# Optimization experiments

Hardware: AMD Instinct MI355X
Metric: run time of the kernel (lower is better)

## Reference

```python
import jax, jax.numpy as jnp
import numpy as np

N_NODES = 50000
N_EDGES = 800000
HIDDEN = 128
STATIC = 16
EDGE_F = 16
HEADS = 8
HEAD_SIZE = HIDDEN // HEADS
MLP_IN = 2 * HIDDEN + 2 * STATIC + EDGE_F  # 304
MLP_WIDTH = 2 * HIDDEN  # 256


def setup_inputs() -> dict:
    key = jax.random.key(0)
    ks = jax.random.split(key, 7)
    h = jax.random.normal(ks[0], (N_NODES, HIDDEN), dtype=jnp.float32)
    x_s = jax.random.normal(ks[1], (N_NODES, STATIC), dtype=jnp.float32)
    edge_index = jax.random.randint(ks[2], (2, N_EDGES), 0, N_NODES, dtype=jnp.int32)
    edge_features = jax.random.normal(ks[3], (N_EDGES, EDGE_F), dtype=jnp.float32)
    W1 = jax.random.normal(ks[4], (MLP_WIDTH, MLP_IN), dtype=jnp.float32) / np.sqrt(MLP_IN)
    W2 = jax.random.normal(ks[5], (HEADS, MLP_WIDTH), dtype=jnp.float32) / np.sqrt(MLP_WIDTH)
    Wout = jax.random.normal(ks[6], (HIDDEN, HIDDEN), dtype=jnp.float32) / np.sqrt(HIDDEN)
    return {"h": h, "x_s": x_s, "edge_index": edge_index,
            "edge_features": edge_features, "W1": W1, "W2": W2, "Wout": Wout}


def reference(h, x_s, edge_index, edge_features, W1, W2, Wout):
    num_nodes, hidden = h.shape
    # original does edge_index[::-1] -> src = edge_index[1], dest = edge_index[0]
    src, dest = edge_index[1], edge_index[0]
    # per-edge gate MLP (depth=1, relu hidden, no bias)
    mlp_input = jnp.concatenate([h[src], h[dest], x_s[src], x_s[dest], edge_features], axis=-1)  # [E, 304]
    hidden_act = jax.nn.relu(mlp_input @ W1.T)          # [E, width]
    raw_scores = hidden_act @ W2.T                      # [E, heads]
    gates = jax.nn.sigmoid(raw_scores)                  # [E, heads]
    # head-split gather-multiply-scatter
    h_heads = h.reshape(num_nodes, HEADS, HEAD_SIZE)
    gated = h_heads[src] * gates[:, :, None]            # [E, heads, head_size]
    agg = jax.ops.segment_sum(gated, dest, num_segments=num_nodes)  # [N, heads, head_size]
    agg = agg.reshape(num_nodes, hidden)
    projected = agg @ Wout.T                            # [N, hidden]
    return (projected, gates)
```

## Files before the change

### kernel.cpp

```cpp
#include <hip/hip_runtime.h>
#include <hip/hip_bf16.h>

#define N_NODES 50000
#define N_EDGES 800000
#define HIDDEN 128
#define STATIC 16
#define EDGE_F 16
#define HEADS 8
#define KIN 304
#define KPAD 320
#define WID 256
#define TILE 64
#define NTILES (N_EDGES / TILE)
#define NB 512

typedef short bf16x8 __attribute__((ext_vector_type(8)));
typedef unsigned short u16x4 __attribute__((ext_vector_type(4)));
typedef unsigned short u16x8 __attribute__((ext_vector_type(8)));
typedef float f32x4 __attribute__((ext_vector_type(4)));

__device__ __forceinline__ unsigned short f2bf(float x) {
    __hip_bfloat16 b = __float2bfloat16(x);
    return __builtin_bit_cast(unsigned short, b);
}

__global__ void prep_weights_kernel(const float* __restrict__ W1,
                                    const float* __restrict__ W2,
                                    unsigned short* __restrict__ wb1p,
                                    unsigned short* __restrict__ wb2p) {
    int gi = blockIdx.x * 256 + threadIdx.x;
    if (gi < WID * (KPAD / 8)) {
        int row = gi / 40, kg = gi - row * 40;
        u16x8 o = (u16x8)0;
        if (kg < 38) {
            const float* s = W1 + (size_t)row * KIN + kg * 8;
            #pragma unroll
            for (int i = 0; i < 8; ++i) o[i] = f2bf(s[i]);
        }
        *(u16x8*)(wb1p + (size_t)gi * 8) = o;
    } else {
        int gj = gi - WID * (KPAD / 8);
        if (gj < 16 * 32) {
            int row = gj >> 5, kg = gj & 31;
            u16x8 o = (u16x8)0;
            if (row < HEADS) {
                const float* s = W2 + (size_t)row * WID + kg * 8;
                #pragma unroll
                for (int i = 0; i < 8; ++i) o[i] = f2bf(s[i]);
            }
            *(u16x8*)(wb2p + (size_t)gj * 8) = o;
        }
    }
}

#define HB_G  (N_NODES * HIDDEN / 8)
#define XSB_G (N_NODES * STATIC / 8)
#define EFB_G (N_EDGES * EDGE_F / 8)
__global__ void prep_data_kernel(const float* __restrict__ h,
                                 const float* __restrict__ xs,
                                 const float* __restrict__ ef,
                                 unsigned short* __restrict__ hb,
                                 unsigned short* __restrict__ xsb,
                                 unsigned short* __restrict__ efb) {
    size_t gi = (size_t)blockIdx.x * 256 + threadIdx.x;
    const float* s;
    unsigned short* d;
    if (gi < HB_G)                    { s = h  + gi * 8;              d = hb  + gi * 8; }
    else if (gi < HB_G + XSB_G)       { size_t k = gi - HB_G;         s = xs + k * 8; d = xsb + k * 8; }
    else if (gi < HB_G + XSB_G + EFB_G) { size_t k = gi - HB_G - XSB_G; s = ef + k * 8; d = efb + k * 8; }
    else return;
    u16x8 o;
    #pragma unroll
    for (int i = 0; i < 8; ++i) o[i] = f2bf(s[i]);
    *(u16x8*)d = o;
}

template <bool PRE>
__global__ __launch_bounds__(256, 2) void mlp_gates_kernel(
    const float* __restrict__ hf, const float* __restrict__ xsf,
    const int* __restrict__ ei, const float* __restrict__ eff,
    const unsigned short* __restrict__ wb1p, const unsigned short* __restrict__ wb2p,
    const unsigned short* __restrict__ hb, const unsigned short* __restrict__ xsb,
    const unsigned short* __restrict__ efb,
    float* __restrict__ gates_out)
{
    __shared__ __align__(16) short A_sh[TILE * KPAD];
    __shared__ __align__(16) short hid_sh[TILE * WID];
    __shared__ int src_s[TILE], dst_s[TILE];

    const int tid  = threadIdx.x;
    const int lane = tid & 63;
    const int w    = tid >> 6;
    const int r    = lane & 15;
    const int g    = lane >> 4;
    const int xorv = (r & 7) << 4;

    bf16x8 b1[4][10];
    #pragma unroll
    for (int t = 0; t < 4; ++t)
        #pragma unroll
        for (int ks = 0; ks < 10; ++ks)
            b1[t][ks] = *(const bf16x8*)(wb1p + (size_t)((w * 4 + t) * 16 + r) * KPAD + ks * 32 + g * 8);
    bf16x8 w2f[8];
    #pragma unroll
    for (int k2 = 0; k2 < 8; ++k2)
        w2f[k2] = *(const bf16x8*)(wb2p + (size_t)r * WID + k2 * 32 + g * 8);

    int tile = blockIdx.x;
    if (tid < TILE && tile < NTILES) {
        src_s[tid] = ei[N_EDGES + tile * TILE + tid];
        dst_s[tid] = ei[tile * TILE + tid];
    }
    __syncthreads();

    for (; tile < NTILES; tile += NB) {
        const int e0 = tile * TILE;

        if (PRE) {
            const u16x8* h8  = (const u16x8*)hb;
            const u16x8* xs8 = (const u16x8*)xsb;
            const u16x8* ef8 = (const u16x8*)efb;
            #pragma unroll
            for (int idx = tid; idx < 1024; idx += 256) {
                int e = idx >> 4, c = idx & 15;
                u16x8 v = h8[(size_t)src_s[e] * 16 + c];
                *(u16x8*)((char*)A_sh + e * 640 + (((c << 4)) ^ ((e & 7) << 4))) = v;
            }
            #pragma unroll
            for (int idx = tid; idx < 1024; idx += 256) {
                int e = idx >> 4, c = idx & 15;
                u16x8 v = h8[(size_t)dst_s[e] * 16 + c];
                *(u16x8*)((char*)A_sh + e * 640 + ((256 + (c << 4)) ^ ((e & 7) << 4))) = v;
            }
            #pragma unroll
            for (int idx = tid; idx < 512; idx += 256) {
                int e = idx >> 3, c = idx & 7;
                u16x8 v = (u16x8)0;
                if (c < 2)      v = xs8[(size_t)src_s[e] * 2 + c];
                else if (c < 4) v = xs8[(size_t)dst_s[e] * 2 + (c - 2)];
                else if (c < 6) v = ef8[(size_t)(e0 + e) * 2 + (c - 4)];
                *(u16x8*)((char*)A_sh + e * 640 + ((512 + (c << 4)) ^ ((e & 7) << 4))) = v;
            }
        } else {
            const float4* h4  = (const float4*)hf;
            const float4* xs4 = (const float4*)xsf;
            const float4* ef4 = (const float4*)eff;
            #pragma unroll
            for (int idx = tid; idx < 2048; idx += 256) {
                int e = idx >> 5, q = idx & 31;
                float4 v = h4[(size_t)src_s[e] * 32 + q];
                u16x4 p; p[0] = f2bf(v.x); p[1] = f2bf(v.y); p[2] = f2bf(v.z); p[3] = f2bf(v.w);
                *(u16x4*)((char*)A_sh + e * 640 + (((q << 3)) ^ ((e & 7) << 4))) = p;
            }
            #pragma unroll
            for (int idx = tid; idx < 2048; idx += 256) {
                int e = idx >> 5, q = idx & 31;
                float4 v = h4[(size_t)dst_s[e] * 32 + q];
                u16x4 p; p[0] = f2bf(v.x); p[1] = f2bf(v.y); p[2] = f2bf(v.z); p[3] = f2bf(v.w);
                *(u16x4*)((char*)A_sh + e * 640 + ((256 + (q << 3)) ^ ((e & 7) << 4))) = p;
            }
            #pragma unroll
            for (int idx = tid; idx < 1024; idx += 256) {
                int e = idx >> 4, c = idx & 15;
                float4 v = make_float4(0.f, 0.f, 0.f, 0.f);
                if (c < 4)       v = xs4[(size_t)src_s[e] * 4 + c];
                else if (c < 8)  v = xs4[(size_t)dst_s[e] * 4 + (c - 4)];
                else if (c < 12) v = ef4[(size_t)(e0 + e) * 4 + (c - 8)];
                u16x4 p; p[0] = f2bf(v.x); p[1] = f2bf(v.y); p[2] = f2bf(v.z); p[3] = f2bf(v.w);
                *(u16x4*)((char*)A_sh + e * 640 + ((512 + (c << 3)) ^ ((e & 7) << 4))) = p;
            }
        }
        __syncthreads();

        int nsrc = 0, ndst = 0;
        const int ntile = tile + NB;
        const bool more = (ntile < NTILES);
        if (tid < TILE && more) {
            nsrc = ei[N_EDGES + ntile * TILE + tid];
            ndst = ei[ntile * TILE + tid];
        }

        #pragma unroll
        for (int sub = 0; sub < 4; ++sub) {
            f32x4 acc[4];
            #pragma unroll
            for (int t = 0; t < 4; ++t) acc[t] = (f32x4)(0.f);
            const char* abase = (const char*)A_sh + (sub * 16 + r) * 640;
            #pragma unroll
            for (int ks = 0; ks < 10; ++ks) {
                bf16x8 a = *(const bf16x8*)(abase + (((ks << 6) | (g << 4)) ^ xorv));
                #pragma unroll
                for (int t = 0; t < 4; ++t)
                    acc[t] = __builtin_amdgcn_mfma_f32_16x16x32_bf16(a, b1[t][ks], acc[t], 0, 0, 0);
            }
            #pragma unroll
            for (int t = 0; t < 4; ++t)
                #pragma unroll
                for (int q = 0; q < 4; ++q) {
                    int e = sub * 16 + g * 4 + q;
                    int n = (w * 4 + t) * 16 + r;
                    *(short*)((char*)hid_sh + e * 512 + ((n * 2) ^ ((e & 7) << 4))) =
                        (short)f2bf(fmaxf(acc[t][q], 0.f));
                }
        }
        if (tid < TILE && more) { src_s[tid] = nsrc; dst_s[tid] = ndst; }
        __syncthreads();

        f32x4 sacc = (f32x4)(0.f);
        const char* hbase = (const char*)hid_sh + (w * 16 + r) * 512;
        #pragma unroll
        for (int k2 = 0; k2 < 8; ++k2) {
            bf16x8 a2 = *(const bf16x8*)(hbase + (((k2 << 6) | (g << 4)) ^ xorv));
            sacc = __builtin_amdgcn_mfma_f32_16x16x32_bf16(a2, w2f[k2], sacc, 0, 0, 0);
        }
        if (r < HEADS) {
            #pragma unroll
            for (int q = 0; q < 4; ++q) {
                int e = e0 + w * 16 + g * 4 + q;
                gates_out[(size_t)e * HEADS + r] = 1.f / (1.f + __expf(-sacc[q]));
            }
        }
    }
}

__global__ void hist_kernel(const int* __restrict__ ei, int* __restrict__ deg) {
    int e = blockIdx.x * 256 + threadIdx.x;
    if (e < N_EDGES) atomicAdd(&deg[ei[e]], 1);
}

#define SCAN_T 1024
#define SCAN_CHUNK 49
__global__ __launch_bounds__(SCAN_T) void scan_kernel(
    const int* __restrict__ deg, int* __restrict__ offs, int* __restrict__ cursor) {
    __shared__ int part[SCAN_T];
    int t = threadIdx.x;
    int b = t * SCAN_CHUNK;
    int s = 0;
    for (int i = 0; i < SCAN_CHUNK; ++i) {
        int idx = b + i;
        if (idx < N_NODES) s += deg[idx];
    }
    part[t] = s;
    __syncthreads();
    for (int off = 1; off < SCAN_T; off <<= 1) {
        int v = (t >= off) ? part[t - off] : 0;
        __syncthreads();
        part[t] += v;
        __syncthreads();
    }
    int run = (t == 0) ? 0 : part[t - 1];
    for (int i = 0; i < SCAN_CHUNK; ++i) {
        int idx = b + i;
        if (idx < N_NODES) {
            int dv = deg[idx];
            offs[idx] = run;
            cursor[idx] = run;
            run += dv;
        }
    }
    if (t == SCAN_T - 1) offs[N_NODES] = run;
}

__global__ void permute_kernel(const int* __restrict__ ei, int* __restrict__ cursor,
                               int* __restrict__ perm) {
    int e = blockIdx.x * 256 + threadIdx.x;
    if (e < N_EDGES) {
        int d = ei[e];
        int pos = atomicAdd(&cursor[d], 1);
        perm[pos] = e;
    }
}

__global__ __launch_bounds__(256) void agg_csr_kernel(
    const float* __restrict__ h, const int* __restrict__ ei,
    const float* __restrict__ gates, const int* __restrict__ offs,
    const int* __restrict__ perm, float* __restrict__ agg)
{
    int d = (blockIdx.x * 256 + threadIdx.x) >> 6;
    if (d >= N_NODES) return;
    int lane = threadIdx.x & 63;
    int f = lane << 1;
    int hsel = f >> 4;
    int beg = offs[d], end = offs[d + 1];
    float ax = 0.f, ay = 0.f;
    for (int j0 = beg; j0 < end; j0 += 64) {
        int cnt = min(64, end - j0);
        int el = 0, sl = 0;
        if (lane < cnt) {
            el = perm[j0 + lane];
            sl = ei[N_EDGES + el];
        }
        for (int i = 0; i < cnt; ++i) {
            int e = __shfl(el, i);
            int s = __shfl(sl, i);
            float gg = gates[(size_t)e * HEADS + hsel];
            float2 v = *(const float2*)(h + (size_t)s * HIDDEN + f);
            ax += v.x * gg;
            ay += v.y * gg;
        }
    }
    float2 o; o.x = ax; o.y = ay;
    *(float2*)(agg + (size_t)d * HIDDEN + f) = o;
}

__global__ __launch_bounds__(256) void scatter_kernel(
    const float* __restrict__ h, const int* __restrict__ ei,
    const float* __restrict__ gates, float* __restrict__ agg)
{
    int gid = blockIdx.x * 256 + threadIdx.x;
    int e  = gid >> 5;
    int f0 = (gid & 31) << 2;
    int s = ei[N_EDGES + e];
    int d = ei[e];
    float g = gates[(size_t)e * HEADS + (f0 >> 4)];
    float4 v = *(const float4*)(h + (size_t)s * HIDDEN + f0);
    float* out = agg + (size_t)d * HIDDEN + f0;
    atomicAdd(out + 0, v.x * g);
    atomicAdd(out + 1, v.y * g);
    atomicAdd(out + 2, v.z * g);
    atomicAdd(out + 3, v.w * g);
}

__global__ __launch_bounds__(256, 1) void proj_kernel(
    const float* __restrict__ Wout, float* __restrict__ out)
{
    __shared__ float wlds[HIDDEN][129];
    __shared__ float aggs[32][HIDDEN];
    const int tid = threadIdx.x;
    const int n0 = blockIdx.x * 32;

    for (int i = tid; i < HIDDEN * HIDDEN; i += 256)
        wlds[i >> 7][i & 127] = Wout[i];
    for (int i = tid; i < 32 * HIDDEN; i += 256) {
        int nl = i >> 7, f = i & 127;
        int n = n0 + nl;
        aggs[nl][f] = (n < N_NODES) ? out[(size_t)n * HIDDEN + f] : 0.f;
    }
    __syncthreads();

    for (int i = 0; i < 16; ++i) {
        int idx = tid + (i << 8);
        int nl = idx >> 7, o = idx & 127;
        float acc = 0.f;
        #pragma unroll 8
        for (int k = 0; k < HIDDEN; ++k) acc += aggs[nl][k] * wlds[o][k];
        int n = n0 + nl;
        if (n < N_NODES) out[(size_t)n * HIDDEN + o] = acc;
    }
}

extern "C" void kernel_launch(void* const* d_in, const int* in_sizes, int n_in,
                              void* d_out, int out_size, void* d_ws, size_t ws_size,
                              hipStream_t stream) {
    const float* h    = (const float*)d_in[0];
    const float* xs   = (const float*)d_in[1];
    const int*   ei   = (const int*)d_in[2];
    const float* ef   = (const float*)d_in[3];
    const float* W1   = (const float*)d_in[4];
    const float* W2   = (const float*)d_in[5];
    const float* Wout = (const float*)d_in[6];

    float* proj_out  = (float*)d_out;
    float* gates_out = proj_out + (size_t)N_NODES * HIDDEN;

    const size_t OFF_WB1  = 0;
    const size_t OFF_WB2  = 163840;
    const size_t OFF_DEG  = 172032;
    const size_t OFF_OFFS = 372096;
    const size_t OFF_CUR  = 572160;
    const size_t OFF_PERM = 772224;
    const size_t OFF_HB   = 3972224;
    const size_t OFF_XSB  = 16772224;
    const size_t OFF_EFB  = 18372224;
    const size_t NEED_FULL = 43972224;
    const size_t NEED_CSR  = 3972224;

    unsigned short* wb1p = (unsigned short*)((char*)d_ws + OFF_WB1);
    unsigned short* wb2p = (unsigned short*)((char*)d_ws + OFF_WB2);
    unsigned short* hbp  = (unsigned short*)((char*)d_ws + OFF_HB);
    unsigned short* xsbp = (unsigned short*)((char*)d_ws + OFF_XSB);
    unsigned short* efbp = (unsigned short*)((char*)d_ws + OFF_EFB);

    const bool pre = ws_size >= NEED_FULL;
    const bool csr = ws_size >= NEED_CSR;

    prep_weights_kernel<<<42, 256, 0, stream>>>(W1, W2, wb1p, wb2p);
    if (pre) {
        prep_data_kernel<<<(HB_G + XSB_G + EFB_G + 255) / 256, 256, 0, stream>>>(
            h, xs, ef, hbp, xsbp, efbp);
        mlp_gates_kernel<true><<<NB, 256, 0, stream>>>(
            h, xs, ei, ef, wb1p, wb2p, hbp, xsbp, efbp, gates_out);
    } else {
        mlp_gates_kernel<false><<<NB, 256, 0, stream>>>(
            h, xs, ei, ef, wb1p, wb2p, hbp, xsbp, efbp, gates_out);
    }

    if (csr) {
        int* deg    = (int*)((char*)d_ws + OFF_DEG);
        int* offs   = (int*)((char*)d_ws + OFF_OFFS);
        int* cursor = (int*)((char*)d_ws + OFF_CUR);
        int* perm   = (int*)((char*)d_ws + OFF_PERM);

        hipMemsetAsync(deg, 0, N_NODES * sizeof(int), stream);
        hist_kernel<<<(N_EDGES + 255) / 256, 256, 0, stream>>>(ei, deg);
        scan_kernel<<<1, SCAN_T, 0, stream>>>(deg, offs, cursor);
        permute_kernel<<<(N_EDGES + 255) / 256, 256, 0, stream>>>(ei, cursor, perm);
        agg_csr_kernel<<<(N_NODES * 64 + 255) / 256, 256, 0, stream>>>(
            h, ei, gates_out, offs, perm, proj_out);
    } else {
        hipMemsetAsync(proj_out, 0, (size_t)N_NODES * HIDDEN * sizeof(float), stream);
        scatter_kernel<<<(N_EDGES * 32) / 256, 256, 0, stream>>>(h, ei, gates_out, proj_out);
    }

    proj_kernel<<<(N_NODES + 31) / 32, 256, 0, stream>>>(Wout, proj_out);
}
```

Before: 1.045 ms.

## Use bf16 for aggregation gathers and projection via MFMA, drop edge-feature prepass

The CSR aggregation now gathers bf16 node features from the prepacked copy, unrolls by four edges to issue more loads at once, and writes the aggregate as bf16 to a workspace buffer. A new MFMA-based projection kernel multiplies that aggregate by a bf16 copy of Wout, replacing the scalar fp32 projection. The separate edge-feature bf16 prepass is removed and edge features are converted inline in the MLP kernel. This cuts memory traffic and the scalar GEMM cost, at the price of extra bf16 rounding on the aggregate and the output weights.

```diff
diff --git a/kernel.cpp b/kernel.cpp
--- a/kernel.cpp
+++ b/kernel.cpp
@@ -23,11 +23,19 @@
     __hip_bfloat16 b = __float2bfloat16(x);
     return __builtin_bit_cast(unsigned short, b);
 }
+__device__ __forceinline__ float bflo(unsigned int v) {
+    return __builtin_bit_cast(float, v << 16);
+}
+__device__ __forceinline__ float bfhi(unsigned int v) {
+    return __builtin_bit_cast(float, v & 0xffff0000u);
+}
 
 __global__ void prep_weights_kernel(const float* __restrict__ W1,
                                     const float* __restrict__ W2,
+                                    const float* __restrict__ Wout,
                                     unsigned short* __restrict__ wb1p,
-                                    unsigned short* __restrict__ wb2p) {
+                                    unsigned short* __restrict__ wb2p,
+                                    unsigned short* __restrict__ wob) {
     int gi = blockIdx.x * 256 + threadIdx.x;
     if (gi < WID * (KPAD / 8)) {
         int row = gi / 40, kg = gi - row * 40;
@@ -38,36 +46,42 @@
             for (int i = 0; i < 8; ++i) o[i] = f2bf(s[i]);
         }
         *(u16x8*)(wb1p + (size_t)gi * 8) = o;
-    } else {
-        int gj = gi - WID * (KPAD / 8);
-        if (gj < 16 * 32) {
-            int row = gj >> 5, kg = gj & 31;
-            u16x8 o = (u16x8)0;
-            if (row < HEADS) {
-                const float* s = W2 + (size_t)row * WID + kg * 8;
-                #pragma unroll
-                for (int i = 0; i < 8; ++i) o[i] = f2bf(s[i]);
-            }
-            *(u16x8*)(wb2p + (size_t)gj * 8) = o;
-        }
+        return;
+    }
+    int gj = gi - WID * (KPAD / 8);
+    if (gj < 512) {
+        int row = gj >> 5, kg = gj & 31;
+        u16x8 o = (u16x8)0;
+        if (row < HEADS) {
+            const float* s = W2 + (size_t)row * WID + kg * 8;
+            #pragma unroll
+            for (int i = 0; i < 8; ++i) o[i] = f2bf(s[i]);
+        }
+        *(u16x8*)(wb2p + (size_t)gj * 8) = o;
+        return;
+    }
+    int gk = gj - 512;
+    if (gk < 2048) {
+        int row = gk >> 4, kg = gk & 15;
+        const float* s = Wout + (size_t)row * HIDDEN + kg * 8;
+        u16x8 o;
+        #pragma unroll
+        for (int i = 0; i < 8; ++i) o[i] = f2bf(s[i]);
+        *(u16x8*)(wob + (size_t)gk * 8) = o;
     }
 }
 
 #define HB_G  (N_NODES * HIDDEN / 8)
 #define XSB_G (N_NODES * STATIC / 8)
-#define EFB_G (N_EDGES * EDGE_F / 8)
 __global__ void prep_data_kernel(const float* __restrict__ h,
                                  const float* __restrict__ xs,
-                                 const float* __restrict__ ef,
                                  unsigned short* __restrict__ hb,
-                                 unsigned short* __restrict__ xsb,
-                                 unsigned short* __restrict__ efb) {
+                                 unsigned short* __restrict__ xsb) {
     size_t gi = (size_t)blockIdx.x * 256 + threadIdx.x;
     const float* s;
     unsigned short* d;
-    if (gi < HB_G)                    { s = h  + gi * 8;              d = hb  + gi * 8; }
-    else if (gi < HB_G + XSB_G)       { size_t k = gi - HB_G;         s = xs + k * 8; d = xsb + k * 8; }
-    else if (gi < HB_G + XSB_G + EFB_G) { size_t k = gi - HB_G - XSB_G; s = ef + k * 8; d = efb + k * 8; }
+    if (gi < HB_G)              { s = h  + gi * 8;        d = hb  + gi * 8; }
+    else if (gi < HB_G + XSB_G) { size_t k = gi - HB_G;   s = xs + k * 8; d = xsb + k * 8; }
     else return;
     u16x8 o;
     #pragma unroll
@@ -76,12 +90,12 @@
 }
 
 template <bool PRE>
-__global__ __launch_bounds__(256, 2) void mlp_gates_kernel(
+__global__ __attribute__((amdgpu_flat_work_group_size(256, 256), amdgpu_waves_per_eu(2, 2)))
+void mlp_gates_kernel(
     const float* __restrict__ hf, const float* __restrict__ xsf,
     const int* __restrict__ ei, const float* __restrict__ eff,
     const unsigned short* __restrict__ wb1p, const unsigned short* __restrict__ wb2p,
     const unsigned short* __restrict__ hb, const unsigned short* __restrict__ xsb,
-    const unsigned short* __restrict__ efb,
     float* __restrict__ gates_out)
 {
     __shared__ __align__(16) short A_sh[TILE * KPAD];
@@ -119,7 +133,6 @@
         if (PRE) {
             const u16x8* h8  = (const u16x8*)hb;
             const u16x8* xs8 = (const u16x8*)xsb;
-            const u16x8* ef8 = (const u16x8*)efb;
             #pragma unroll
             for (int idx = tid; idx < 1024; idx += 256) {
                 int e = idx >> 4, c = idx & 15;
@@ -138,7 +151,12 @@
                 u16x8 v = (u16x8)0;
                 if (c < 2)      v = xs8[(size_t)src_s[e] * 2 + c];
                 else if (c < 4) v = xs8[(size_t)dst_s[e] * 2 + (c - 2)];
-                else if (c < 6) v = ef8[(size_t)(e0 + e) * 2 + (c - 4)];
+                else if (c < 6) {
+                    const float4* p = (const float4*)(eff + (size_t)(e0 + e) * EDGE_F + (c - 4) * 8);
+                    float4 v0 = p[0], v1 = p[1];
+                    v[0] = f2bf(v0.x); v[1] = f2bf(v0.y); v[2] = f2bf(v0.z); v[3] = f2bf(v0.w);
+                    v[4] = f2bf(v1.x); v[5] = f2bf(v1.y); v[6] = f2bf(v1.z); v[7] = f2bf(v1.w);
+                }
                 *(u16x8*)((char*)A_sh + e * 640 + ((512 + (c << 4)) ^ ((e & 7) << 4))) = v;
             }
         } else {
@@ -272,9 +290,9 @@
 }
 
 __global__ __launch_bounds__(256) void agg_csr_kernel(
-    const float* __restrict__ h, const int* __restrict__ ei,
+    const unsigned short* __restrict__ hb, const int* __restrict__ ei,
     const float* __restrict__ gates, const int* __restrict__ offs,
-    const int* __restrict__ perm, float* __restrict__ agg)
+    const int* __restrict__ perm, unsigned short* __restrict__ aggb)
 {
     int d = (blockIdx.x * 256 + threadIdx.x) >> 6;
     if (d >= N_NODES) return;
@@ -290,17 +308,82 @@
             el = perm[j0 + lane];
             sl = ei[N_EDGES + el];
         }
-        for (int i = 0; i < cnt; ++i) {
+        int i = 0;
+        for (; i + 4 <= cnt; i += 4) {
+            float gv[4];
+            unsigned int hv[4];
+            #pragma unroll
+            for (int k = 0; k < 4; ++k) {
+                int e = __shfl(el, i + k);
+                int s = __shfl(sl, i + k);
+                gv[k] = gates[(size_t)e * HEADS + hsel];
+                hv[k] = *(const unsigned int*)(hb + (size_t)s * HIDDEN + f);
+            }
+            #pragma unroll
+            for (int k = 0; k < 4; ++k) {
+                ax += bflo(hv[k]) * gv[k];
+                ay += bfhi(hv[k]) * gv[k];
+            }
+        }
+        for (; i < cnt; ++i) {
             int e = __shfl(el, i);
             int s = __shfl(sl, i);
             float gg = gates[(size_t)e * HEADS + hsel];
-            float2 v = *(const float2*)(h + (size_t)s * HIDDEN + f);
-            ax += v.x * gg;
-            ay += v.y * gg;
-        }
-    }
-    float2 o; o.x = ax; o.y = ay;
-    *(float2*)(agg + (size_t)d * HIDDEN + f) = o;
+            unsigned int hv = *(const unsigned int*)(hb + (size_t)s * HIDDEN + f);
+            ax += bflo(hv) * gg;
+            ay += bfhi(hv) * gg;
+        }
+    }
+    unsigned int o = ((unsigned int)f2bf(ay) << 16) | (unsigned int)f2bf(ax);
+    *(unsigned int*)(aggb + (size_t)d * HIDDEN + f) = o;
+}
+
+__global__ __launch_bounds__(256) void proj_mfma_kernel(
+    const unsigned short* __restrict__ aggb, const unsigned short* __restrict__ wob,
+    float* __restrict__ out)
+{
+    __shared__ __align__(16) short A_sh[64 * 128];
+    const int tid = threadIdx.x, lane = tid & 63, w = tid >> 6;
+    const int r = lane & 15, g = lane >> 4;
+    const int xorv = (r & 7) << 4;
+    const int n0 = blockIdx.x * 64;
+
+    bf16x8 b[2][4];
+    #pragma unroll
+    for (int t = 0; t < 2; ++t)
+        #pragma unroll
+        for (int ks = 0; ks < 4; ++ks)
+            b[t][ks] = *(const bf16x8*)(wob + (size_t)((w * 2 + t) * 16 + r) * HIDDEN + ks * 32 + g * 8);
+
+    for (int idx = tid; idx < 1024; idx += 256) {
+        int e = idx >> 4, c = idx & 15;
+        int n = n0 + e;
+        u16x8 v = (u16x8)0;
+        if (n < N_NODES) v = *(const u16x8*)(aggb + (size_t)n * HIDDEN + c * 8);
+        *(u16x8*)((char*)A_sh + e * 256 + ((c << 4) ^ ((e & 7) << 4))) = v;
+    }
+    __syncthreads();
+
+    #pragma unroll
+    for (int sub = 0; sub < 4; ++sub) {
+        f32x4 acc[2];
+        acc[0] = (f32x4)(0.f); acc[1] = (f32x4)(0.f);
+        const char* abase = (const char*)A_sh + (sub * 16 + r) * 256;
+        #pragma unroll
+        for (int ks = 0; ks < 4; ++ks) {
+            bf16x8 a = *(const bf16x8*)(abase + (((ks << 6) | (g << 4)) ^ xorv));
+            acc[0] = __builtin_amdgcn_mfma_f32_16x16x32_bf16(a, b[0][ks], acc[0], 0, 0, 0);
+            acc[1] = __builtin_amdgcn_mfma_f32_16x16x32_bf16(a, b[1][ks], acc[1], 0, 0, 0);
+        }
+        #pragma unroll
+        for (int t = 0; t < 2; ++t)
+            #pragma unroll
+            for (int q = 0; q < 4; ++q) {
+                int n = n0 + sub * 16 + g * 4 + q;
+                if (n < N_NODES)
+                    out[(size_t)n * HIDDEN + (w * 2 + t) * 16 + r] = acc[t][q];
+            }
+    }
 }
 
 __global__ __launch_bounds__(256) void scatter_kernel(
@@ -365,52 +448,47 @@
 
     const size_t OFF_WB1  = 0;
     const size_t OFF_WB2  = 163840;
-    const size_t OFF_DEG  = 172032;
-    const size_t OFF_OFFS = 372096;
-    const size_t OFF_CUR  = 572160;
-    const size_t OFF_PERM = 772224;
-    const size_t OFF_HB   = 3972224;
-    const size_t OFF_XSB  = 16772224;
-    const size_t OFF_EFB  = 18372224;
-    const size_t NEED_FULL = 43972224;
-    const size_t NEED_CSR  = 3972224;
+    const size_t OFF_WOB  = 172032;
+    const size_t OFF_DEG  = 204800;
+    const size_t OFF_OFFS = 405504;
+    const size_t OFF_CUR  = 606208;
+    const size_t OFF_PERM = 806912;
+    const size_t OFF_AGGB = 4006912;
+    const size_t OFF_HB   = 16806912;
+    const size_t OFF_XSB  = 29606912;
+    const size_t NEED_FULL = 31206912;
 
     unsigned short* wb1p = (unsigned short*)((char*)d_ws + OFF_WB1);
     unsigned short* wb2p = (unsigned short*)((char*)d_ws + OFF_WB2);
+    unsigned short* wob  = (unsigned short*)((char*)d_ws + OFF_WOB);
+    unsigned short* aggb = (unsigned short*)((char*)d_ws + OFF_AGGB);
     unsigned short* hbp  = (unsigned short*)((char*)d_ws + OFF_HB);
     unsigned short* xsbp = (unsigned short*)((char*)d_ws + OFF_XSB);
-    unsigned short* efbp = (unsigned short*)((char*)d_ws + OFF_EFB);
-
-    const bool pre = ws_size >= NEED_FULL;
-    const bool csr = ws_size >= NEED_CSR;
-
-    prep_weights_kernel<<<42, 256, 0, stream>>>(W1, W2, wb1p, wb2p);
-    if (pre) {
-        prep_data_kernel<<<(HB_G + XSB_G + EFB_G + 255) / 256, 256, 0, stream>>>(
-            h, xs, ef, hbp, xsbp, efbp);
-        mlp_gates_kernel<true><<<NB, 256, 0, stream>>>(
-            h, xs, ei, ef, wb1p, wb2p, hbp, xsbp, efbp, gates_out);
-    } else {
-        mlp_gates_kernel<false><<<NB, 256, 0, stream>>>(
-            h, xs, ei, ef, wb1p, wb2p, hbp, xsbp, efbp, gates_out);
-    }
-
-    if (csr) {
+
+    prep_weights_kernel<<<50, 256, 0, stream>>>(W1, W2, Wout, wb1p, wb2p, wob);
+
+    if (ws_size >= NEED_FULL) {
         int* deg    = (int*)((char*)d_ws + OFF_DEG);
         int* offs   = (int*)((char*)d_ws + OFF_OFFS);
         int* cursor = (int*)((char*)d_ws + OFF_CUR);
         int* perm   = (int*)((char*)d_ws + OFF_PERM);
+
+        prep_data_kernel<<<(HB_G + XSB_G + 255) / 256, 256, 0, stream>>>(h, xs, hbp, xsbp);
+        mlp_gates_kernel<true><<<NB, 256, 0, stream>>>(
+            h, xs, ei, ef, wb1p, wb2p, hbp, xsbp, gates_out);
 
         hipMemsetAsync(deg, 0, N_NODES * sizeof(int), stream);
         hist_kernel<<<(N_EDGES + 255) / 256, 256, 0, stream>>>(ei, deg);
         scan_kernel<<<1, SCAN_T, 0, stream>>>(deg, offs, cursor);
         permute_kernel<<<(N_EDGES + 255) / 256, 256, 0, stream>>>(ei, cursor, perm);
         agg_csr_kernel<<<(N_NODES * 64 + 255) / 256, 256, 0, stream>>>(
-            h, ei, gates_out, offs, perm, proj_out);
+            hbp, ei, gates_out, offs, perm, aggb);
+        proj_mfma_kernel<<<(N_NODES + 63) / 64, 256, 0, stream>>>(aggb, wob, proj_out);
     } else {
+        mlp_gates_kernel<false><<<NB, 256, 0, stream>>>(
+            h, xs, ei, ef, wb1p, wb2p, nullptr, nullptr, gates_out);
         hipMemsetAsync(proj_out, 0, (size_t)N_NODES * HIDDEN * sizeof(float), stream);
         scatter_kernel<<<(N_EDGES * 32) / 256, 256, 0, stream>>>(h, ei, gates_out, proj_out);
-    }
-
-    proj_kernel<<<(N_NODES + 31) / 32, 256, 0, stream>>>(Wout, proj_out);
-}
+        proj_kernel<<<(N_NODES + 31) / 32, 256, 0, stream>>>(Wout, proj_out);
+    }
+}
```

Result: faster. 849.6 us (-18.7%).
